# Performance work log

Hardware: AMD Instinct MI355X
Metric: run time of the kernel (lower is better)

Reference implementation:

```python
import jax, jax.numpy as jnp
import numpy as np

T, B, I, H = 512, 64, 512, 512

def setup_inputs() -> dict:
    key = jax.random.key(0)
    ks = jax.random.split(key, 7)
    s_in = 1.0 / np.sqrt(H)
    return {
        "input": jax.random.normal(ks[0], (T, B, I), dtype=jnp.float32),
        "h0": jax.random.normal(ks[1], (B, H), dtype=jnp.float32),
        "c0": jax.random.normal(ks[2], (B, H), dtype=jnp.float32),
        "W_ih": jax.random.uniform(ks[3], (4 * H, I), dtype=jnp.float32, minval=-s_in, maxval=s_in),
        "W_hh": jax.random.uniform(ks[4], (4 * H, H), dtype=jnp.float32, minval=-s_in, maxval=s_in),
        "b_ih": jax.random.uniform(ks[5], (4 * H,), dtype=jnp.float32, minval=-s_in, maxval=s_in),
        "b_hh": jax.random.uniform(ks[6], (4 * H,), dtype=jnp.float32, minval=-s_in, maxval=s_in),
    }

def reference(input, h0, c0, W_ih, W_hh, b_ih, b_hh):
    # Precompute input projections for all timesteps: [T, B, 4H]
    x_proj = jnp.einsum('tbi,gi->tbg', input, W_ih) + b_ih + b_hh

    def step(state, xp):
        h, c = state
        gates = xp + h @ W_hh.T  # [B, 4H]
        i_g, f_g, g_g, o_g = jnp.split(gates, 4, axis=-1)
        i_g = jax.nn.sigmoid(i_g)
        f_g = jax.nn.sigmoid(f_g)
        g_g = jnp.tanh(g_g)
        o_g = jax.nn.sigmoid(o_g)
        c_new = f_g * c + i_g * g_g
        h_new = o_g * jnp.tanh(c_new)
        return (h_new, c_new), h_new

    # reverse=True: process last timestep first, outputs placed at original indices
    (h_f, c_f), outputs = jax.lax.scan(step, (h0, c0), x_proj, reverse=True)
    return outputs, h_f, c_f
```

## Files before the change

kernel.cpp:

```cpp
#include <hip/hip_runtime.h>
#include <math.h>
#include <stdint.h>

#define T_ 512
#define B_ 64
#define I_ 512
#define H_ 512
#define G_ 2048
#define K_ 1024
#define NMR 32
#define NCOL 4
#define NBLK (NMR * NCOL)

typedef __bf16 bf16x8 __attribute__((ext_vector_type(8)));
typedef float f32x4 __attribute__((ext_vector_type(4)));
typedef int i32x4 __attribute__((ext_vector_type(4)));

#define OFF_W    ((size_t)0)
#define OFF_BIAS (OFF_W + (size_t)G_ * K_ * 2)
#define OFF_HSWZ (OFF_BIAS + (size_t)G_ * 4)
#define OFF_BAR  (OFF_HSWZ + (size_t)2 * H_ * B_ * 2)
#define OFF_XSWZ (OFF_BAR + 1024)


__global__ void prep_w(const float* __restrict__ W_ih, const float* __restrict__ W_hh,
                       const float* __restrict__ b_ih, const float* __restrict__ b_hh,
                       char* __restrict__ ws) {
    __bf16* W = (__bf16*)(ws + OFF_W);
    float* bias = (float*)(ws + OFF_BIAS);
    int idx = blockIdx.x * 256 + threadIdx.x;
    int g = idx >> 10;
    int k = idx & (K_ - 1);
    float v = (k < I_) ? W_ih[g * I_ + k] : W_hh[g * H_ + (k - I_)];
    W[idx] = (__bf16)v;
    if (idx < G_) bias[idx] = b_ih[idx] + b_hh[idx];
    if (idx < 256) ((unsigned*)(ws + OFF_BAR))[idx] = 0u;
}

__global__ void prep_x(const float* __restrict__ input, char* __restrict__ ws) {
    __bf16* xswz = (__bf16*)(ws + OFF_XSWZ);
    int s = blockIdx.x * 256 + threadIdx.x;
    int lane = s & 63;
    int nblk = (s >> 6) & 3;
    int kblk = (s >> 8) & 15;
    int t = s >> 12;
    int b = nblk * 16 + (lane & 15);
    int k = kblk * 32 + (lane >> 4) * 8;
    const float* src = input + ((size_t)t * B_ + b) * I_ + k;
    float4 v0 = *(const float4*)src;
    float4 v1 = *(const float4*)(src + 4);
    bf16x8 o;
    o[0]=(__bf16)v0.x; o[1]=(__bf16)v0.y; o[2]=(__bf16)v0.z; o[3]=(__bf16)v0.w;
    o[4]=(__bf16)v1.x; o[5]=(__bf16)v1.y; o[6]=(__bf16)v1.z; o[7]=(__bf16)v1.w;
    *(bf16x8*)(xswz + (size_t)s * 8) = o;
}

__global__ void prep_h0(const float* __restrict__ h0, char* __restrict__ ws) {
    __bf16* hswz0 = (__bf16*)(ws + OFF_HSWZ);
    int s = blockIdx.x * 256 + threadIdx.x;
    int lane = s & 63;
    int nblk = (s >> 6) & 3;
    int hk = s >> 8;
    int b = nblk * 16 + (lane & 15);
    int u = hk * 32 + (lane >> 4) * 8;
    const float* src = h0 + (size_t)b * H_ + u;
    float4 v0 = *(const float4*)src;
    float4 v1 = *(const float4*)(src + 4);
    bf16x8 o;
    o[0]=(__bf16)v0.x; o[1]=(__bf16)v0.y; o[2]=(__bf16)v0.z; o[3]=(__bf16)v0.w;
    o[4]=(__bf16)v1.x; o[5]=(__bf16)v1.y; o[6]=(__bf16)v1.z; o[7]=(__bf16)v1.w;
    *(bf16x8*)(hswz0 + (size_t)s * 8) = o;
}

__device__ __forceinline__ float sigmoid_f(float x) { return 1.f / (1.f + __expf(-x)); }
__device__ __forceinline__ float tanh_f(float x) { return 1.f - 2.f / (1.f + __expf(2.f * x)); }

__launch_bounds__(256, 1)
__global__ void lstm_persist(const float* __restrict__ c0, float* out,
                             char* __restrict__ ws) {
    __shared__ __bf16 xbuf[8192];
    __shared__ __bf16 hbuf[8192];
    __shared__ float gl[4][16][17];
    __shared__ __bf16 hstage[2][16][8];

    const __bf16* W = (const __bf16*)(ws + OFF_W);
    const float* bias = (const float*)(ws + OFF_BIAS);
    __bf16* Hswz = (__bf16*)(ws + OFF_HSWZ);
    const __bf16* Xswz = (const __bf16*)(ws + OFF_XSWZ);
    unsigned* flags = (unsigned*)(ws + OFF_BAR);

    const int tid = threadIdx.x;
    const int wave = tid >> 6;
    const int lane = tid & 63;
    const int l16 = lane & 15;
    const int quad = lane >> 4;
    const int wgM = blockIdx.x & 31;
    const int wgN = blockIdx.x >> 5;

    bf16x8 A[32];
    {
        const size_t arow = (size_t)(wave * H_ + wgM * 16 + l16) * K_ + quad * 8;
        #pragma unroll
        for (int ks = 0; ks < 32; ++ks)
            A[ks] = *(const bf16x8*)(W + arow + ks * 32);
    }

    const int cu_u = tid & 15;
    const int cu_bl = tid >> 4;
    const int hu = wgM * 16 + cu_u;
    const int batch = wgN * 16 + cu_bl;
    float creg = c0[(size_t)batch * H_ + hu];
    const float bias_i = bias[hu];
    const float bias_f = bias[H_ + hu];
    const float bias_g = bias[2 * H_ + hu];
    const float bias_o = bias[3 * H_ + hu];

    {
        const __bf16* xb = Xswz + (size_t)(T_ - 1) * 32768;
        #pragma unroll
        for (int i = 0; i < 4; ++i) {
            const int kb = wave * 4 + i;
            __builtin_amdgcn_global_load_lds(
                (const __attribute__((address_space(1))) void*)(xb + (size_t)((kb * 4 + wgN) * 64 + lane) * 8),
                (__attribute__((address_space(3))) void*)(xbuf + kb * 512),
                16, 0, 0);
        }
    }

    for (int t = T_ - 1; ; --t) {
        if (t < T_ - 1) {
            if (tid < 64) {
                const unsigned target = (unsigned)(T_ - 1 - t);
                const unsigned long long faddr =
                    (unsigned long long)(uintptr_t)(flags + wgN * 64 + (lane & 31));
                unsigned cur;
                do {
                    asm volatile("global_load_dword %0, %1, off sc0 sc1\n\t"
                                 "s_waitcnt vmcnt(0)"
                                 : "=v"(cur) : "v"(faddr) : "memory");
                } while (!__all(lane >= 32 || cur >= target));
            }
            __syncthreads();
        }

        {
            const __bf16* hb = Hswz + (size_t)((t + 1) & 1) * 32768;
            #pragma unroll
            for (int i = 0; i < 4; ++i) {
                const int hk = wave * 4 + i;
                __builtin_amdgcn_global_load_lds(
                    (const __attribute__((address_space(1))) void*)(hb + (size_t)((hk * 4 + wgN) * 64 + lane) * 8),
                    (__attribute__((address_space(3))) void*)(hbuf + hk * 512),
                    16, 0, 0x11);
            }
        }
        asm volatile("s_waitcnt vmcnt(4)" ::: "memory");
        __syncthreads();

        f32x4 acc = {0, 0, 0, 0};
        #pragma unroll
        for (int f = 0; f < 16; ++f) {
            bf16x8 b = *(const bf16x8*)(xbuf + f * 512 + lane * 8);
            acc = __builtin_amdgcn_mfma_f32_16x16x32_bf16(A[f], b, acc, 0, 0, 0);
        }
        asm volatile("s_waitcnt vmcnt(0)" ::: "memory");
        __syncthreads();

        #pragma unroll
        for (int f = 0; f < 16; ++f) {
            bf16x8 b = *(const bf16x8*)(hbuf + f * 512 + lane * 8);
            acc = __builtin_amdgcn_mfma_f32_16x16x32_bf16(A[16 + f], b, acc, 0, 0, 0);
        }

        #pragma unroll
        for (int r = 0; r < 4; ++r)
            gl[wave][quad * 4 + r][l16] = acc[r];
        __syncthreads();

        float ig = sigmoid_f(gl[0][cu_u][cu_bl] + bias_i);
        float fg = sigmoid_f(gl[1][cu_u][cu_bl] + bias_f);
        float gg = tanh_f(gl[2][cu_u][cu_bl] + bias_g);
        float og = sigmoid_f(gl[3][cu_u][cu_bl] + bias_o);
        float cn = fg * creg + ig * gg;
        creg = cn;
        float hn = og * tanh_f(cn);
        hstage[cu_u >> 3][cu_bl][cu_u & 7] = (__bf16)hn;
        __syncthreads();

        if (t != 0) {
            if (tid < 32) {
                i32x4 v = *(i32x4*)((__bf16*)hstage + tid * 8);
                const int lqc = tid >> 4, l16c = tid & 15;
                const int hk = wgM >> 1, q0 = (wgM & 1) * 2;
                size_t off = (size_t)((hk * 4 + wgN) * 64 + (q0 + lqc) * 16 + l16c) * 8;
                __bf16* dst = Hswz + (size_t)(t & 1) * 32768 + off;
                asm volatile("global_store_dwordx4 %0, %1, off sc0 sc1"
                             :: "v"(dst), "v"(v) : "memory");
            }
            asm volatile("s_waitcnt vmcnt(0)" ::: "memory");
            if (tid == 0) {
                const unsigned val = (unsigned)(T_ - t);
                const unsigned long long faddr =
                    (unsigned long long)(uintptr_t)(flags + wgN * 64 + wgM);
                asm volatile("global_store_dword %0, %1, off sc0 sc1"
                             :: "v"(faddr), "v"(val) : "memory");
            }
        }

        out[(size_t)t * B_ * H_ + (size_t)batch * H_ + hu] = hn;
        if (t == 0) {
            out[(size_t)T_ * B_ * H_ + (size_t)batch * H_ + hu] = hn;
            out[(size_t)T_ * B_ * H_ + B_ * H_ + (size_t)batch * H_ + hu] = cn;
            break;
        }

        {
            const __bf16* xb = Xswz + (size_t)(t - 1) * 32768;
            #pragma unroll
            for (int i = 0; i < 4; ++i) {
                const int kb = wave * 4 + i;
                __builtin_amdgcn_global_load_lds(
                    (const __attribute__((address_space(1))) void*)(xb + (size_t)((kb * 4 + wgN) * 64 + lane) * 8),
                    (__attribute__((address_space(3))) void*)(xbuf + kb * 512),
                    16, 0, 0);
            }
        }
    }
}

extern "C" void kernel_launch(void* const* d_in, const int* in_sizes, int n_in,
                              void* d_out, int out_size, void* d_ws, size_t ws_size,
                              hipStream_t stream) {
    const float* input = (const float*)d_in[0];
    const float* h0   = (const float*)d_in[1];
    const float* c0   = (const float*)d_in[2];
    const float* W_ih = (const float*)d_in[3];
    const float* W_hh = (const float*)d_in[4];
    const float* b_ih = (const float*)d_in[5];
    const float* b_hh = (const float*)d_in[6];
    float* out = (float*)d_out;
    char* ws = (char*)d_ws;

    prep_w<<<(G_ * K_) / 256, 256, 0, stream>>>(W_ih, W_hh, b_ih, b_hh, ws);
    prep_x<<<(T_ * I_ * B_ / 8) / 256, 256, 0, stream>>>(input, ws);
    prep_h0<<<16, 256, 0, stream>>>(h0, ws);
    lstm_persist<<<NBLK, 256, 0, stream>>>(c0, out, ws);
}
```

Baseline: 1.562 ms.

## Per-wave flag synchronization with per-wave full h loads and split MFMA accumulators

Replaces the block-wide spin barrier with per-wave flags: each wave publishes its own slice of h and a flag, then polls all 32 producer groups' flags with dwordx4 loads. Each wave then loads the full h vector into a private LDS buffer, staged with partial vmcnt waits so MFMAs can start before all of h arrives. This removes most __syncthreads. Accumulation is split into four independent MFMA chains to hide MFMA latency, and the gate buffer is double-buffered by timestep parity. The cost is four times the h-load traffic and LDS use, plus more flag polling traffic.

```diff
diff --git a/kernel.cpp b/kernel.cpp
--- a/kernel.cpp
+++ b/kernel.cpp
@@ -20,7 +20,7 @@
 #define OFF_BIAS (OFF_W + (size_t)G_ * K_ * 2)
 #define OFF_HSWZ (OFF_BIAS + (size_t)G_ * 4)
 #define OFF_BAR  (OFF_HSWZ + (size_t)2 * H_ * B_ * 2)
-#define OFF_XSWZ (OFF_BAR + 1024)
+#define OFF_XSWZ (OFF_BAR + 2048)
 
 
 __global__ void prep_w(const float* __restrict__ W_ih, const float* __restrict__ W_hh,
@@ -34,7 +34,7 @@
     float v = (k < I_) ? W_ih[g * I_ + k] : W_hh[g * H_ + (k - I_)];
     W[idx] = (__bf16)v;
     if (idx < G_) bias[idx] = b_ih[idx] + b_hh[idx];
-    if (idx < 256) ((unsigned*)(ws + OFF_BAR))[idx] = 0u;
+    if (idx < 512) ((unsigned*)(ws + OFF_BAR))[idx] = 0u;
 }
 
 __global__ void prep_x(const float* __restrict__ input, char* __restrict__ ws) {
@@ -78,10 +78,10 @@
 __launch_bounds__(256, 1)
 __global__ void lstm_persist(const float* __restrict__ c0, float* out,
                              char* __restrict__ ws) {
-    __shared__ __bf16 xbuf[8192];
-    __shared__ __bf16 hbuf[8192];
-    __shared__ float gl[4][16][17];
-    __shared__ __bf16 hstage[2][16][8];
+    __shared__ __attribute__((aligned(16))) __bf16 xbuf[8192];
+    __shared__ __attribute__((aligned(16))) __bf16 hbuf[4][8192];
+    __shared__ float gl[2][4][16][17];
+    __shared__ __attribute__((aligned(16))) __bf16 hsc[4][64];
 
     const __bf16* W = (const __bf16*)(ws + OFF_W);
     const float* bias = (const float*)(ws + OFF_BIAS);
@@ -115,117 +115,174 @@
     const float bias_g = bias[2 * H_ + hu];
     const float bias_o = bias[3 * H_ + hu];
 
-    {
-        const __bf16* xb = Xswz + (size_t)(T_ - 1) * 32768;
+    #define ISSUE_X(tt) do {                                                          \
+        const __bf16* xb_ = Xswz + (size_t)(tt) * 32768;                              \
+        _Pragma("unroll")                                                             \
+        for (int i_ = 0; i_ < 4; ++i_) {                                              \
+            const int kb_ = wave * 4 + i_;                                            \
+            __builtin_amdgcn_global_load_lds(                                         \
+                (const __attribute__((address_space(1))) void*)(xb_ + (size_t)((kb_ * 4 + wgN) * 64 + lane) * 8), \
+                (__attribute__((address_space(3))) void*)(xbuf + kb_ * 512),          \
+                16, 0, 0);                                                            \
+        }                                                                             \
+    } while (0)
+
+    #define ISSUE_H(par) do {                                                         \
+        const __bf16* hb_ = Hswz + (size_t)(par) * 32768;                             \
+        _Pragma("unroll")                                                             \
+        for (int f_ = 0; f_ < 16; ++f_) {                                             \
+            __builtin_amdgcn_global_load_lds(                                         \
+                (const __attribute__((address_space(1))) void*)(hb_ + (size_t)((f_ * 4 + wgN) * 64 + lane) * 8), \
+                (__attribute__((address_space(3))) void*)(hbuf[wave] + f_ * 512),     \
+                16, 0, 0x11);                                                         \
+        }                                                                             \
+    } while (0)
+
+    ISSUE_X(T_ - 1);
+    ISSUE_H(0);
+    asm volatile("s_waitcnt vmcnt(16)" ::: "memory");
+    __builtin_amdgcn_sched_barrier(0);
+
+    for (int t = T_ - 1; ; --t) {
+        __builtin_amdgcn_s_barrier();
+        __builtin_amdgcn_sched_barrier(0);
+
+        f32x4 ac0 = {0,0,0,0}, ac1 = {0,0,0,0}, ac2 = {0,0,0,0}, ac3 = {0,0,0,0};
         #pragma unroll
-        for (int i = 0; i < 4; ++i) {
-            const int kb = wave * 4 + i;
-            __builtin_amdgcn_global_load_lds(
-                (const __attribute__((address_space(1))) void*)(xb + (size_t)((kb * 4 + wgN) * 64 + lane) * 8),
-                (__attribute__((address_space(3))) void*)(xbuf + kb * 512),
-                16, 0, 0);
-        }
-    }
-
-    for (int t = T_ - 1; ; --t) {
-        if (t < T_ - 1) {
-            if (tid < 64) {
-                const unsigned target = (unsigned)(T_ - 1 - t);
-                const unsigned long long faddr =
-                    (unsigned long long)(uintptr_t)(flags + wgN * 64 + (lane & 31));
-                unsigned cur;
-                do {
-                    asm volatile("global_load_dword %0, %1, off sc0 sc1\n\t"
-                                 "s_waitcnt vmcnt(0)"
-                                 : "=v"(cur) : "v"(faddr) : "memory");
-                } while (!__all(lane >= 32 || cur >= target));
-            }
-            __syncthreads();
-        }
-
-        {
-            const __bf16* hb = Hswz + (size_t)((t + 1) & 1) * 32768;
-            #pragma unroll
-            for (int i = 0; i < 4; ++i) {
-                const int hk = wave * 4 + i;
-                __builtin_amdgcn_global_load_lds(
-                    (const __attribute__((address_space(1))) void*)(hb + (size_t)((hk * 4 + wgN) * 64 + lane) * 8),
-                    (__attribute__((address_space(3))) void*)(hbuf + hk * 512),
-                    16, 0, 0x11);
-            }
+        for (int f = 0; f < 4; ++f) {
+            bf16x8 b0 = *(const bf16x8*)(xbuf + (4*f+0) * 512 + lane * 8);
+            bf16x8 b1 = *(const bf16x8*)(xbuf + (4*f+1) * 512 + lane * 8);
+            bf16x8 b2 = *(const bf16x8*)(xbuf + (4*f+2) * 512 + lane * 8);
+            bf16x8 b3 = *(const bf16x8*)(xbuf + (4*f+3) * 512 + lane * 8);
+            ac0 = __builtin_amdgcn_mfma_f32_16x16x32_bf16(A[4*f+0], b0, ac0, 0, 0, 0);
+            ac1 = __builtin_amdgcn_mfma_f32_16x16x32_bf16(A[4*f+1], b1, ac1, 0, 0, 0);
+            ac2 = __builtin_amdgcn_mfma_f32_16x16x32_bf16(A[4*f+2], b2, ac2, 0, 0, 0);
+            ac3 = __builtin_amdgcn_mfma_f32_16x16x32_bf16(A[4*f+3], b3, ac3, 0, 0, 0);
+        }
+
+        const __bf16* hwb = hbuf[wave];
+        asm volatile("s_waitcnt vmcnt(12)" ::: "memory");
+        {
+            bf16x8 b0 = *(const bf16x8*)(hwb + 0*512 + lane*8);
+            bf16x8 b1 = *(const bf16x8*)(hwb + 1*512 + lane*8);
+            bf16x8 b2 = *(const bf16x8*)(hwb + 2*512 + lane*8);
+            bf16x8 b3 = *(const bf16x8*)(hwb + 3*512 + lane*8);
+            ac0 = __builtin_amdgcn_mfma_f32_16x16x32_bf16(A[16], b0, ac0, 0, 0, 0);
+            ac1 = __builtin_amdgcn_mfma_f32_16x16x32_bf16(A[17], b1, ac1, 0, 0, 0);
+            ac2 = __builtin_amdgcn_mfma_f32_16x16x32_bf16(A[18], b2, ac2, 0, 0, 0);
+            ac3 = __builtin_amdgcn_mfma_f32_16x16x32_bf16(A[19], b3, ac3, 0, 0, 0);
+        }
+        asm volatile("s_waitcnt vmcnt(8)" ::: "memory");
+        {
+            bf16x8 b0 = *(const bf16x8*)(hwb + 4*512 + lane*8);
+            bf16x8 b1 = *(const bf16x8*)(hwb + 5*512 + lane*8);
+            bf16x8 b2 = *(const bf16x8*)(hwb + 6*512 + lane*8);
+            bf16x8 b3 = *(const bf16x8*)(hwb + 7*512 + lane*8);
+            ac0 = __builtin_amdgcn_mfma_f32_16x16x32_bf16(A[20], b0, ac0, 0, 0, 0);
+            ac1 = __builtin_amdgcn_mfma_f32_16x16x32_bf16(A[21], b1, ac1, 0, 0, 0);
+            ac2 = __builtin_amdgcn_mfma_f32_16x16x32_bf16(A[22], b2, ac2, 0, 0, 0);
+            ac3 = __builtin_amdgcn_mfma_f32_16x16x32_bf16(A[23], b3, ac3, 0, 0, 0);
         }
         asm volatile("s_waitcnt vmcnt(4)" ::: "memory");
-        __syncthreads();
-
-        f32x4 acc = {0, 0, 0, 0};
-        #pragma unroll
-        for (int f = 0; f < 16; ++f) {
-            bf16x8 b = *(const bf16x8*)(xbuf + f * 512 + lane * 8);
-            acc = __builtin_amdgcn_mfma_f32_16x16x32_bf16(A[f], b, acc, 0, 0, 0);
+        {
+            bf16x8 b0 = *(const bf16x8*)(hwb + 8*512 + lane*8);
+            bf16x8 b1 = *(const bf16x8*)(hwb + 9*512 + lane*8);
+            bf16x8 b2 = *(const bf16x8*)(hwb + 10*512 + lane*8);
+            bf16x8 b3 = *(const bf16x8*)(hwb + 11*512 + lane*8);
+            ac0 = __builtin_amdgcn_mfma_f32_16x16x32_bf16(A[24], b0, ac0, 0, 0, 0);
+            ac1 = __builtin_amdgcn_mfma_f32_16x16x32_bf16(A[25], b1, ac1, 0, 0, 0);
+            ac2 = __builtin_amdgcn_mfma_f32_16x16x32_bf16(A[26], b2, ac2, 0, 0, 0);
+            ac3 = __builtin_amdgcn_mfma_f32_16x16x32_bf16(A[27], b3, ac3, 0, 0, 0);
         }
         asm volatile("s_waitcnt vmcnt(0)" ::: "memory");
-        __syncthreads();
-
-        #pragma unroll
-        for (int f = 0; f < 16; ++f) {
-            bf16x8 b = *(const bf16x8*)(hbuf + f * 512 + lane * 8);
-            acc = __builtin_amdgcn_mfma_f32_16x16x32_bf16(A[16 + f], b, acc, 0, 0, 0);
-        }
-
+        {
+            bf16x8 b0 = *(const bf16x8*)(hwb + 12*512 + lane*8);
+            bf16x8 b1 = *(const bf16x8*)(hwb + 13*512 + lane*8);
+            bf16x8 b2 = *(const bf16x8*)(hwb + 14*512 + lane*8);
+            bf16x8 b3 = *(const bf16x8*)(hwb + 15*512 + lane*8);
+            ac0 = __builtin_amdgcn_mfma_f32_16x16x32_bf16(A[28], b0, ac0, 0, 0, 0);
+            ac1 = __builtin_amdgcn_mfma_f32_16x16x32_bf16(A[29], b1, ac1, 0, 0, 0);
+            ac2 = __builtin_amdgcn_mfma_f32_16x16x32_bf16(A[30], b2, ac2, 0, 0, 0);
+            ac3 = __builtin_amdgcn_mfma_f32_16x16x32_bf16(A[31], b3, ac3, 0, 0, 0);
+        }
+
+        f32x4 accT = (ac0 + ac1) + (ac2 + ac3);
+
+        const int p = t & 1;
         #pragma unroll
         for (int r = 0; r < 4; ++r)
-            gl[wave][quad * 4 + r][l16] = acc[r];
+            gl[p][wave][quad * 4 + r][l16] = accT[r];
         __syncthreads();
 
-        float ig = sigmoid_f(gl[0][cu_u][cu_bl] + bias_i);
-        float fg = sigmoid_f(gl[1][cu_u][cu_bl] + bias_f);
-        float gg = tanh_f(gl[2][cu_u][cu_bl] + bias_g);
-        float og = sigmoid_f(gl[3][cu_u][cu_bl] + bias_o);
+        const float vgi = gl[p][0][cu_u][cu_bl];
+        const float vgf = gl[p][1][cu_u][cu_bl];
+        const float vgg = gl[p][2][cu_u][cu_bl];
+        const float vgo = gl[p][3][cu_u][cu_bl];
+
+        float ig = sigmoid_f(vgi + bias_i);
+        float fg = sigmoid_f(vgf + bias_f);
+        float gg = tanh_f(vgg + bias_g);
+        float og = sigmoid_f(vgo + bias_o);
         float cn = fg * creg + ig * gg;
         creg = cn;
         float hn = og * tanh_f(cn);
-        hstage[cu_u >> 3][cu_bl][cu_u & 7] = (__bf16)hn;
-        __syncthreads();
-
-        if (t != 0) {
-            if (tid < 32) {
-                i32x4 v = *(i32x4*)((__bf16*)hstage + tid * 8);
-                const int lqc = tid >> 4, l16c = tid & 15;
-                const int hk = wgM >> 1, q0 = (wgM & 1) * 2;
-                size_t off = (size_t)((hk * 4 + wgN) * 64 + (q0 + lqc) * 16 + l16c) * 8;
-                __bf16* dst = Hswz + (size_t)(t & 1) * 32768 + off;
-                asm volatile("global_store_dwordx4 %0, %1, off sc0 sc1"
-                             :: "v"(dst), "v"(v) : "memory");
-            }
-            asm volatile("s_waitcnt vmcnt(0)" ::: "memory");
-            if (tid == 0) {
-                const unsigned val = (unsigned)(T_ - t);
-                const unsigned long long faddr =
-                    (unsigned long long)(uintptr_t)(flags + wgN * 64 + wgM);
-                asm volatile("global_store_dword %0, %1, off sc0 sc1"
-                             :: "v"(faddr), "v"(val) : "memory");
-            }
-        }
-
-        out[(size_t)t * B_ * H_ + (size_t)batch * H_ + hu] = hn;
+
         if (t == 0) {
+            out[(size_t)batch * H_ + hu] = hn;
             out[(size_t)T_ * B_ * H_ + (size_t)batch * H_ + hu] = hn;
             out[(size_t)T_ * B_ * H_ + B_ * H_ + (size_t)batch * H_ + hu] = cn;
             break;
         }
 
-        {
-            const __bf16* xb = Xswz + (size_t)(t - 1) * 32768;
-            #pragma unroll
-            for (int i = 0; i < 4; ++i) {
-                const int kb = wave * 4 + i;
-                __builtin_amdgcn_global_load_lds(
-                    (const __attribute__((address_space(1))) void*)(xb + (size_t)((kb * 4 + wgN) * 64 + lane) * 8),
-                    (__attribute__((address_space(3))) void*)(xbuf + kb * 512),
-                    16, 0, 0);
+        const unsigned tgt = (unsigned)(T_ - t);
+
+        hsc[wave][lane] = (__bf16)hn;
+        asm volatile("s_waitcnt lgkmcnt(0)" ::: "memory");
+        __builtin_amdgcn_sched_barrier(0);
+        if (lane < 8) {
+            const int lb = lane >> 1, qr = lane & 1;
+            i32x4 hv = *(const i32x4*)(&hsc[wave][lb * 16 + qr * 8]);
+            const int q = (wgM & 1) * 2 + qr;
+            const int l16c = wave * 4 + lb;
+            __bf16* dst = Hswz + (size_t)(t & 1) * 32768 +
+                (size_t)(((wgM >> 1) * 4 + wgN) * 64 + q * 16 + l16c) * 8;
+            asm volatile("global_store_dwordx4 %0, %1, off sc0 sc1"
+                         :: "v"(dst), "v"(hv) : "memory");
+        }
+        asm volatile("s_waitcnt vmcnt(0)" ::: "memory");
+        if (lane == 0) {
+            const unsigned long long myf = (unsigned long long)(uintptr_t)
+                (flags + wgN * 128 + wgM * 4 + wave);
+            asm volatile("global_store_dword %0, %1, off sc0 sc1"
+                         :: "v"(myf), "v"(tgt) : "memory");
+        }
+
+        out[(size_t)t * B_ * H_ + (size_t)batch * H_ + hu] = hn;
+        ISSUE_X(t - 1);
+
+        {
+            const unsigned long long faddr = (unsigned long long)(uintptr_t)
+                (flags + wgN * 128 + (lane & 31) * 4);
+            i32x4 f4;
+            asm volatile("global_load_dwordx4 %0, %1, off sc0 sc1\n\t"
+                         "s_waitcnt vmcnt(0)"
+                         : "=v"(f4) : "v"(faddr) : "memory");
+            for (;;) {
+                if ((lane & 31) == wgM) f4[wave] = (int)tgt;
+                int m01 = f4[0] < f4[1] ? f4[0] : f4[1];
+                int m23 = f4[2] < f4[3] ? f4[2] : f4[3];
+                int m = m01 < m23 ? m01 : m23;
+                if (__all(m >= (int)tgt)) break;
+                asm volatile("global_load_dwordx4 %0, %1, off sc0 sc1\n\t"
+                             "s_waitcnt vmcnt(0)"
+                             : "=v"(f4) : "v"(faddr) : "memory");
             }
         }
+
+        ISSUE_H(t & 1);
     }
+    #undef ISSUE_X
+    #undef ISSUE_H
 }
 
 extern "C" void kernel_launch(void* const* d_in, const int* in_sizes, int n_in,
```

New measurement: 2.210 ms. 1.41x slower.

## Restructure recurrent step sync, split MFMA accumulators, reorder x prefetch before h publish

Applied to the files above, without the earlier changes.

Reworks the per-timestep schedule of the persistent LSTM kernel. The flag poll now runs on a different wave and skips the block's own flag. The x-tile prefetch is issued before the h store and flag publish, so it is waited on together with them, and the step-start barrier becomes a raw s_barrier guarded by sched_barrier. The MFMA chain is split into four independent accumulators to break the dependent accumulate chain. One __syncthreads between the x and h phases is dropped, which shortens the critical path but relies on the vmcnt(0) wait in the publish step to keep the x data ready.

```diff
diff --git a/kernel.cpp b/kernel.cpp
--- a/kernel.cpp
+++ b/kernel.cpp
@@ -115,33 +115,37 @@
     const float bias_g = bias[2 * H_ + hu];
     const float bias_o = bias[3 * H_ + hu];
 
-    {
-        const __bf16* xb = Xswz + (size_t)(T_ - 1) * 32768;
-        #pragma unroll
-        for (int i = 0; i < 4; ++i) {
-            const int kb = wave * 4 + i;
-            __builtin_amdgcn_global_load_lds(
-                (const __attribute__((address_space(1))) void*)(xb + (size_t)((kb * 4 + wgN) * 64 + lane) * 8),
-                (__attribute__((address_space(3))) void*)(xbuf + kb * 512),
-                16, 0, 0);
-        }
-    }
+    #define ISSUE_X(tt) do {                                                          \
+        const __bf16* xb_ = Xswz + (size_t)(tt) * 32768;                              \
+        _Pragma("unroll")                                                             \
+        for (int i_ = 0; i_ < 4; ++i_) {                                              \
+            const int kb_ = wave * 4 + i_;                                            \
+            __builtin_amdgcn_global_load_lds(                                         \
+                (const __attribute__((address_space(1))) void*)(xb_ + (size_t)((kb_ * 4 + wgN) * 64 + lane) * 8), \
+                (__attribute__((address_space(3))) void*)(xbuf + kb_ * 512),          \
+                16, 0, 0);                                                            \
+        }                                                                             \
+    } while (0)
+
+    ISSUE_X(T_ - 1);
+    asm volatile("s_waitcnt vmcnt(0)" ::: "memory");
+    __builtin_amdgcn_sched_barrier(0);
 
     for (int t = T_ - 1; ; --t) {
-        if (t < T_ - 1) {
-            if (tid < 64) {
-                const unsigned target = (unsigned)(T_ - 1 - t);
-                const unsigned long long faddr =
-                    (unsigned long long)(uintptr_t)(flags + wgN * 64 + (lane & 31));
-                unsigned cur;
-                do {
-                    asm volatile("global_load_dword %0, %1, off sc0 sc1\n\t"
-                                 "s_waitcnt vmcnt(0)"
-                                 : "=v"(cur) : "v"(faddr) : "memory");
-                } while (!__all(lane >= 32 || cur >= target));
-            }
-            __syncthreads();
-        }
+        if (t < T_ - 1 && wave == 1) {
+            const unsigned target = (unsigned)(T_ - 1 - t);
+            const unsigned long long faddr =
+                (unsigned long long)(uintptr_t)(flags + wgN * 64 + (lane & 31));
+            unsigned cur;
+            do {
+                asm volatile("global_load_dword %0, %1, off sc0 sc1\n\t"
+                             "s_waitcnt vmcnt(0)"
+                             : "=v"(cur) : "v"(faddr) : "memory");
+            } while (!__all(lane >= 32 || lane == wgM || cur >= target));
+        }
+        __builtin_amdgcn_sched_barrier(0);
+        __builtin_amdgcn_s_barrier();
+        __builtin_amdgcn_sched_barrier(0);
 
         {
             const __bf16* hb = Hswz + (size_t)((t + 1) & 1) * 32768;
@@ -154,27 +158,41 @@
                     16, 0, 0x11);
             }
         }
-        asm volatile("s_waitcnt vmcnt(4)" ::: "memory");
-        __syncthreads();
-
-        f32x4 acc = {0, 0, 0, 0};
-        #pragma unroll
-        for (int f = 0; f < 16; ++f) {
-            bf16x8 b = *(const bf16x8*)(xbuf + f * 512 + lane * 8);
-            acc = __builtin_amdgcn_mfma_f32_16x16x32_bf16(A[f], b, acc, 0, 0, 0);
-        }
+
+        f32x4 ac0 = {0,0,0,0}, ac1 = {0,0,0,0}, ac2 = {0,0,0,0}, ac3 = {0,0,0,0};
+        #pragma unroll
+        for (int f = 0; f < 4; ++f) {
+            bf16x8 b0 = *(const bf16x8*)(xbuf + (4*f+0) * 512 + lane * 8);
+            bf16x8 b1 = *(const bf16x8*)(xbuf + (4*f+1) * 512 + lane * 8);
+            bf16x8 b2 = *(const bf16x8*)(xbuf + (4*f+2) * 512 + lane * 8);
+            bf16x8 b3 = *(const bf16x8*)(xbuf + (4*f+3) * 512 + lane * 8);
+            ac0 = __builtin_amdgcn_mfma_f32_16x16x32_bf16(A[4*f+0], b0, ac0, 0, 0, 0);
+            ac1 = __builtin_amdgcn_mfma_f32_16x16x32_bf16(A[4*f+1], b1, ac1, 0, 0, 0);
+            ac2 = __builtin_amdgcn_mfma_f32_16x16x32_bf16(A[4*f+2], b2, ac2, 0, 0, 0);
+            ac3 = __builtin_amdgcn_mfma_f32_16x16x32_bf16(A[4*f+3], b3, ac3, 0, 0, 0);
+        }
+
         asm volatile("s_waitcnt vmcnt(0)" ::: "memory");
-        __syncthreads();
-
-        #pragma unroll
-        for (int f = 0; f < 16; ++f) {
-            bf16x8 b = *(const bf16x8*)(hbuf + f * 512 + lane * 8);
-            acc = __builtin_amdgcn_mfma_f32_16x16x32_bf16(A[16 + f], b, acc, 0, 0, 0);
-        }
+        __builtin_amdgcn_sched_barrier(0);
+        __builtin_amdgcn_s_barrier();
+        __builtin_amdgcn_sched_barrier(0);
+
+        #pragma unroll
+        for (int f = 0; f < 4; ++f) {
+            bf16x8 b0 = *(const bf16x8*)(hbuf + (4*f+0) * 512 + lane * 8);
+            bf16x8 b1 = *(const bf16x8*)(hbuf + (4*f+1) * 512 + lane * 8);
+            bf16x8 b2 = *(const bf16x8*)(hbuf + (4*f+2) * 512 + lane * 8);
+            bf16x8 b3 = *(const bf16x8*)(hbuf + (4*f+3) * 512 + lane * 8);
+            ac0 = __builtin_amdgcn_mfma_f32_16x16x32_bf16(A[16+4*f+0], b0, ac0, 0, 0, 0);
+            ac1 = __builtin_amdgcn_mfma_f32_16x16x32_bf16(A[16+4*f+1], b1, ac1, 0, 0, 0);
+            ac2 = __builtin_amdgcn_mfma_f32_16x16x32_bf16(A[16+4*f+2], b2, ac2, 0, 0, 0);
+            ac3 = __builtin_amdgcn_mfma_f32_16x16x32_bf16(A[16+4*f+3], b3, ac3, 0, 0, 0);
+        }
+        f32x4 accT = (ac0 + ac1) + (ac2 + ac3);
 
         #pragma unroll
         for (int r = 0; r < 4; ++r)
-            gl[wave][quad * 4 + r][l16] = acc[r];
+            gl[wave][quad * 4 + r][l16] = accT[r];
         __syncthreads();
 
         float ig = sigmoid_f(gl[0][cu_u][cu_bl] + bias_i);
@@ -187,45 +205,32 @@
         hstage[cu_u >> 3][cu_bl][cu_u & 7] = (__bf16)hn;
         __syncthreads();
 
-        if (t != 0) {
-            if (tid < 32) {
-                i32x4 v = *(i32x4*)((__bf16*)hstage + tid * 8);
-                const int lqc = tid >> 4, l16c = tid & 15;
-                const int hk = wgM >> 1, q0 = (wgM & 1) * 2;
-                size_t off = (size_t)((hk * 4 + wgN) * 64 + (q0 + lqc) * 16 + l16c) * 8;
-                __bf16* dst = Hswz + (size_t)(t & 1) * 32768 + off;
-                asm volatile("global_store_dwordx4 %0, %1, off sc0 sc1"
-                             :: "v"(dst), "v"(v) : "memory");
-            }
-            asm volatile("s_waitcnt vmcnt(0)" ::: "memory");
-            if (tid == 0) {
-                const unsigned val = (unsigned)(T_ - t);
-                const unsigned long long faddr =
-                    (unsigned long long)(uintptr_t)(flags + wgN * 64 + wgM);
-                asm volatile("global_store_dword %0, %1, off sc0 sc1"
-                             :: "v"(faddr), "v"(val) : "memory");
-            }
-        }
-
         out[(size_t)t * B_ * H_ + (size_t)batch * H_ + hu] = hn;
         if (t == 0) {
             out[(size_t)T_ * B_ * H_ + (size_t)batch * H_ + hu] = hn;
             out[(size_t)T_ * B_ * H_ + B_ * H_ + (size_t)batch * H_ + hu] = cn;
             break;
         }
-
-        {
-            const __bf16* xb = Xswz + (size_t)(t - 1) * 32768;
-            #pragma unroll
-            for (int i = 0; i < 4; ++i) {
-                const int kb = wave * 4 + i;
-                __builtin_amdgcn_global_load_lds(
-                    (const __attribute__((address_space(1))) void*)(xb + (size_t)((kb * 4 + wgN) * 64 + lane) * 8),
-                    (__attribute__((address_space(3))) void*)(xbuf + kb * 512),
-                    16, 0, 0);
-            }
+        ISSUE_X(t - 1);
+        if (tid < 32) {
+            i32x4 v = *(i32x4*)((__bf16*)hstage + tid * 8);
+            const int lqc = tid >> 4, l16c = tid & 15;
+            const int hk = wgM >> 1, q0 = (wgM & 1) * 2;
+            size_t off = (size_t)((hk * 4 + wgN) * 64 + (q0 + lqc) * 16 + l16c) * 8;
+            __bf16* dst = Hswz + (size_t)(t & 1) * 32768 + off;
+            asm volatile("global_store_dwordx4 %0, %1, off sc0 sc1"
+                         :: "v"(dst), "v"(v) : "memory");
+        }
+        asm volatile("s_waitcnt vmcnt(0)" ::: "memory");
+        if (tid == 0) {
+            const unsigned val = (unsigned)(T_ - t);
+            const unsigned long long faddr =
+                (unsigned long long)(uintptr_t)(flags + wgN * 64 + wgM);
+            asm volatile("global_store_dword %0, %1, off sc0 sc1"
+                         :: "v"(faddr), "v"(val) : "memory");
         }
     }
+    #undef ISSUE_X
 }
 
 extern "C" void kernel_launch(void* const* d_in, const int* in_sizes, int n_in,
```

Result: slower. 1.674 ms (+7.2%).
